# Kernel tuning notes

Hardware: AMD Instinct MI355X
Metric: run time of the kernel (lower is better)

Reference implementation:

```python
import jax, jax.numpy as jnp
import numpy as np

V, D, T_MAX, H, L = 32000, 1024, 1024, 16, 8
HD = D // H
DFF = 4 * D
EPS = 1e-5


def _pos_encoding(T, d_model, dtype=jnp.float32):
    pos = jnp.arange(T, dtype=jnp.float32)[:, None]                      # [T,1]
    div = jnp.exp(jnp.arange(0, d_model, 2, dtype=jnp.float32) * (-jnp.log(10000.0) / d_model))
    pe = jnp.zeros((T, d_model), dtype=jnp.float32)
    pe = pe.at[:, 0::2].set(jnp.sin(pos * div))
    pe = pe.at[:, 1::2].set(jnp.cos(pos * div))
    return pe.astype(dtype)


def _layernorm(x, g, b):
    mu = jnp.mean(x, axis=-1, keepdims=True)
    var = jnp.mean(jnp.square(x - mu), axis=-1, keepdims=True)
    return (x - mu) * jax.lax.rsqrt(var + EPS) * g + b


def setup_inputs() -> dict:
    key = jax.random.key(0)
    ks = jax.random.split(key, 9)
    s = 0.02
    return {
        "idx": jax.random.randint(ks[0], (2, 1024), 0, V),
        "embed": jax.random.normal(ks[1], (V, D), jnp.float32) * s,
        "Wqkv": jax.random.normal(ks[2], (L, D, 3 * D), jnp.float32) * s,
        "Wproj": jax.random.normal(ks[3], (L, D, D), jnp.float32) * s,
        "bproj": jnp.zeros((L, D), jnp.float32),
        "ln1_g": jnp.ones((L, D), jnp.float32),
        "ln1_b": jnp.zeros((L, D), jnp.float32),
        "ln2_g": jnp.ones((L, D), jnp.float32),
        "ln2_b": jnp.zeros((L, D), jnp.float32),
        "W1": jax.random.normal(ks[4], (L, D, DFF), jnp.float32) * s,
        "b1": jnp.zeros((L, DFF), jnp.float32),
        "W2": jax.random.normal(ks[5], (L, DFF, D), jnp.float32) * s,
        "b2": jnp.zeros((L, D), jnp.float32),
        "lnf_g": jnp.ones((D,), jnp.float32),
        "lnf_b": jnp.zeros((D,), jnp.float32),
        "Whead": jax.random.normal(ks[6], (D, V), jnp.float32) * s,
    }


def _attn(x, Wqkv, Wproj, bproj):
    B, T, C = x.shape
    qkv = (x @ Wqkv).reshape(B, T, 3, H, HD)
    q, k, v = [jnp.transpose(qkv[:, :, i], (0, 2, 1, 3)) for i in range(3)]  # [B,H,T,HD]
    scores = jnp.einsum('bhqd,bhkd->bhqk', q, k) * (HD ** -0.5)
    mask = jnp.tril(jnp.ones((T, T), dtype=bool))
    scores = jnp.where(mask, scores, -jnp.inf)
    w = jax.nn.softmax(scores, axis=-1)
    out = jnp.einsum('bhqk,bhkd->bhqd', w, v)
    out = jnp.transpose(out, (0, 2, 1, 3)).reshape(B, T, C)
    return out @ Wproj + bproj


def reference(idx, embed, Wqkv, Wproj, bproj, ln1_g, ln1_b, ln2_g, ln2_b,
              W1, b1, W2, b2, lnf_g, lnf_b, Whead):
    idx = idx[:, :T_MAX]
    T = idx.shape[1]
    x = embed[idx] + _pos_encoding(T, D)[None]          # [B,T,D]
    for l in range(L):
        x = x + _attn(_layernorm(x, ln1_g[l], ln1_b[l]), Wqkv[l], Wproj[l], bproj[l])
        h = _layernorm(x, ln2_g[l], ln2_b[l])
        x = x + jax.nn.relu(h @ W1[l] + b1[l]) @ W2[l] + b2[l]
    x = _layernorm(x, lnf_g, lnf_b)
    return x @ Whead                                     # [B,T,V]
```

## Files before the change

kernel.cpp:

```cpp
#include <hip/hip_runtime.h>
#include <cstddef>

#define DM    1024
#define TSEQ  1024
#define NB    2
#define NHEAD 16
#define HDIM  64
#define NLAYER 8
#define DFFN  4096
#define NVOC  32000
#define NROWS (NB*TSEQ)

typedef __attribute__((ext_vector_type(8))) short short8;
typedef __attribute__((ext_vector_type(4))) float f32x4;

static __device__ __forceinline__ unsigned short f2bf(float f) {
    union { float f; unsigned int u; } v; v.f = f;
    unsigned int r = v.u + 0x7FFF + ((v.u >> 16) & 1);
    return (unsigned short)(r >> 16);
}

static __device__ __forceinline__ void gload_lds16(const void* g, void* l) {
    __builtin_amdgcn_global_load_lds(
        (const __attribute__((address_space(1))) unsigned int*)g,
        (__attribute__((address_space(3))) unsigned int*)l, 16, 0, 0);
}

__global__ __launch_bounds__(256)
void embed_pos_k(const int* __restrict__ idx, const float* __restrict__ embed,
                 float* __restrict__ x)
{
    int row = blockIdx.x;
    int t   = row & (TSEQ - 1);
    int tid = threadIdx.x;
    int token = idx[row];
    const float* er = embed + (size_t)token * DM;
    float* xr = x + (size_t)row * DM;
    const float neg_ln1e4_over_d = -9.210340371976184f / (float)DM;
    for (int i = tid; i < DM; i += 256) {
        int half = i >> 1;
        float div = expf((float)(2 * half) * neg_ln1e4_over_d);
        float ang = (float)t * div;
        float pe = (i & 1) ? cosf(ang) : sinf(ang);
        xr[i] = er[i] + pe;
    }
}

__global__ __launch_bounds__(256)
void layernorm_k(const float* __restrict__ x, const float* __restrict__ g,
                 const float* __restrict__ b, unsigned short* __restrict__ y)
{
    int row = blockIdx.x;
    int tid = threadIdx.x;
    const float* xr = x + (size_t)row * DM;
    unsigned short* yr = y + (size_t)row * DM;
    float vals[4];
    float s = 0.f;
    #pragma unroll
    for (int i = 0; i < 4; ++i) { vals[i] = xr[tid + 256 * i]; s += vals[i]; }
    __shared__ float red[256];
    red[tid] = s; __syncthreads();
    for (int st = 128; st > 0; st >>= 1) {
        if (tid < st) red[tid] += red[tid + st];
        __syncthreads();
    }
    float mu = red[0] * (1.f / DM);
    __syncthreads();
    float v = 0.f;
    #pragma unroll
    for (int i = 0; i < 4; ++i) { float d = vals[i] - mu; v += d * d; }
    red[tid] = v; __syncthreads();
    for (int st = 128; st > 0; st >>= 1) {
        if (tid < st) red[tid] += red[tid + st];
        __syncthreads();
    }
    float rstd = rsqrtf(red[0] * (1.f / DM) + 1e-5f);
    #pragma unroll
    for (int i = 0; i < 4; ++i) {
        int c = tid + 256 * i;
        yr[c] = f2bf((vals[i] - mu) * rstd * g[c] + b[c]);
    }
}

__global__ __launch_bounds__(256)
void reduce_ln_k(const float* __restrict__ P, int nsplit, const float* __restrict__ bias,
                 float* __restrict__ X, const float* __restrict__ g,
                 const float* __restrict__ b, unsigned short* __restrict__ XN)
{
    const int row = blockIdx.x;
    const int tid = threadIdx.x;
    const size_t off4 = (size_t)row * 256 + tid;
    const size_t tot4 = (size_t)NROWS * 256;

    float4 v = *((const float4*)X + off4);
    float4 bb = *((const float4*)bias + tid);
    v.x += bb.x; v.y += bb.y; v.z += bb.z; v.w += bb.w;
    for (int s = 0; s < nsplit; ++s) {
        float4 p = *((const float4*)P + s * tot4 + off4);
        v.x += p.x; v.y += p.y; v.z += p.z; v.w += p.w;
    }
    *((float4*)X + off4) = v;

    __shared__ float red[256];
    red[tid] = v.x + v.y + v.z + v.w;
    __syncthreads();
    for (int st = 128; st > 0; st >>= 1) {
        if (tid < st) red[tid] += red[tid + st];
        __syncthreads();
    }
    float mu = red[0] * (1.f / DM);
    __syncthreads();
    float4 d = make_float4(v.x - mu, v.y - mu, v.z - mu, v.w - mu);
    red[tid] = d.x * d.x + d.y * d.y + d.z * d.z + d.w * d.w;
    __syncthreads();
    for (int st = 128; st > 0; st >>= 1) {
        if (tid < st) red[tid] += red[tid + st];
        __syncthreads();
    }
    float rstd = rsqrtf(red[0] * (1.f / DM) + 1e-5f);
    float4 gg = *((const float4*)g + tid);
    float4 bbn = *((const float4*)b + tid);
    unsigned short o[4];
    o[0] = f2bf(d.x * rstd * gg.x + bbn.x);
    o[1] = f2bf(d.y * rstd * gg.y + bbn.y);
    o[2] = f2bf(d.z * rstd * gg.z + bbn.z);
    o[3] = f2bf(d.w * rstd * gg.w + bbn.w);
    *(ushort4*)(XN + (size_t)row * DM + tid * 4) = *(ushort4*)o;
}

__global__ __launch_bounds__(256)
void convt_k(const float* __restrict__ src, unsigned short* __restrict__ dst,
             int K, int N)
{
    __shared__ __align__(16) unsigned short T[64][72];
    const int tid = threadIdx.x;
    const int n0 = blockIdx.x * 64, k0 = blockIdx.y * 64;
    const float* s = src + (size_t)blockIdx.z * K * N;
    unsigned short* d = dst + (size_t)blockIdx.z * K * N;
    #pragma unroll
    for (int q = 0; q < 4; ++q) {
        int f4 = tid + q * 256;
        int kk = f4 >> 4, nn = (f4 & 15) * 4;
        float4 v = *(const float4*)(s + (size_t)(k0 + kk) * N + n0 + nn);
        int swz = ((nn >> 2) & 7) << 3;
        T[nn + 0][kk ^ swz] = f2bf(v.x);
        T[nn + 1][kk ^ swz] = f2bf(v.y);
        T[nn + 2][kk ^ swz] = f2bf(v.z);
        T[nn + 3][kk ^ swz] = f2bf(v.w);
    }
    __syncthreads();
    #pragma unroll
    for (int q = 0; q < 2; ++q) {
        int s8 = tid + q * 256;
        int nn = s8 >> 3, kc = (s8 & 7) * 8;
        int swz = ((nn >> 2) & 7) << 3;
        *(short8*)(d + (size_t)(n0 + nn) * K + k0 + kc) =
            *(const short8*)&T[nn][kc ^ swz];
    }
}

template<bool OUT_BF16>
__global__ __launch_bounds__(512)
void gemm256(const unsigned short* __restrict__ A, const unsigned short* __restrict__ BT,
             const float* __restrict__ bias, void* __restrict__ Cout,
             int M, int N, int K, int relu)
{
    __shared__ __align__(16) unsigned short AS[3][256][64];
    __shared__ __align__(16) unsigned short BS[3][128][64];

    const int tid  = threadIdx.x;
    const int lane = tid & 63;
    const int w    = tid >> 6;
    const int wm = w >> 1, wn = w & 1;
    const int l16 = lane & 15, g = lane >> 4;

    const int nby = M / 256;
    const int nwg = nby * (N / 128);
    const int cpx = nwg >> 3;
    const int bid = (int)blockIdx.x;
    const int sbid = (bid & 7) * cpx + (bid >> 3);
    const int row0 = (sbid % nby) * 256;
    const int col0 = (sbid / nby) * 128;

    const int srow = tid >> 3;
    const int schunk = ((tid & 7) ^ (srow & 7)) << 3;
    const unsigned short* ga = A  + (size_t)(row0 + srow) * K + schunk;
    const unsigned short* gb = BT + (size_t)(col0 + srow) * K + schunk;
    const int NT = K >> 6;

    f32x4 acc[4][4] = {};

    #pragma unroll
    for (int t = 0; t < 2; ++t) {
        #pragma unroll
        for (int i = 0; i < 4; ++i)
            gload_lds16(ga + t * 64 + (size_t)(i * 64) * K,
                        (unsigned short*)AS[t] + i * 4096 + tid * 8);
        #pragma unroll
        for (int i = 0; i < 2; ++i)
            gload_lds16(gb + t * 64 + (size_t)(i * 64) * K,
                        (unsigned short*)BS[t] + i * 4096 + tid * 8);
    }
    asm volatile("s_waitcnt vmcnt(6)" ::: "memory");
    __builtin_amdgcn_s_barrier();

    for (int t = 0; t < NT; ++t) {
        const int rs = t % 3;
        if (t + 2 < NT) {
            const int ss = (t + 2) % 3;
            #pragma unroll
            for (int i = 0; i < 4; ++i)
                gload_lds16(ga + (t + 2) * 64 + (size_t)(i * 64) * K,
                            (unsigned short*)AS[ss] + i * 4096 + tid * 8);
            #pragma unroll
            for (int i = 0; i < 2; ++i)
                gload_lds16(gb + (t + 2) * 64 + (size_t)(i * 64) * K,
                            (unsigned short*)BS[ss] + i * 4096 + tid * 8);
        }
        #pragma unroll
        for (int s = 0; s < 2; ++s) {
            short8 af[4], bf[4];
            #pragma unroll
            for (int i = 0; i < 4; ++i) {
                const int ar = wm * 64 + i * 16 + l16;
                af[i] = *(const short8*)&AS[rs][ar][((((s << 2) | g) ^ (l16 & 7)) << 3)];
            }
            #pragma unroll
            for (int j = 0; j < 4; ++j) {
                const int br = wn * 64 + j * 16 + l16;
                bf[j] = *(const short8*)&BS[rs][br][((((s << 2) | g) ^ (l16 & 7)) << 3)];
            }
            __builtin_amdgcn_s_setprio(1);
            #pragma unroll
            for (int i = 0; i < 4; ++i)
                #pragma unroll
                for (int j = 0; j < 4; ++j)
                    acc[i][j] = __builtin_amdgcn_mfma_f32_16x16x32_bf16(af[i], bf[j], acc[i][j], 0, 0, 0);
            __builtin_amdgcn_s_setprio(0);
        }
        if (t + 2 < NT) { asm volatile("s_waitcnt vmcnt(6)" ::: "memory"); }
        else            { asm volatile("s_waitcnt vmcnt(0)" ::: "memory"); }
        __builtin_amdgcn_s_barrier();
    }

    #pragma unroll
    for (int i = 0; i < 4; ++i) {
        #pragma unroll
        for (int j = 0; j < 4; ++j) {
            #pragma unroll
            for (int r = 0; r < 4; ++r) {
                int row = row0 + wm * 64 + i * 16 + g * 4 + r;
                int col = col0 + wn * 64 + j * 16 + l16;
                float v = acc[i][j][r];
                if (bias) v += bias[col];
                if (relu) v = fmaxf(v, 0.f);
                if (OUT_BF16) ((unsigned short*)Cout)[(size_t)row * N + col] = f2bf(v);
                else          ((float*)Cout)[(size_t)row * N + col] = v;
            }
        }
    }
}

template<int BM, bool OUT_BF16>
__global__ __launch_bounds__(256)
void gemm_tn(const unsigned short* __restrict__ A, const unsigned short* __restrict__ BT,
             const float* __restrict__ bias, const float* __restrict__ residual,
             void* __restrict__ Cout, int M, int N, int K, int KS, int relu)
{
    constexpr int FR = BM / 32;
    constexpr int RPW = BM / 4;
    constexpr int NI = BM / 64;
    __shared__ __align__(16) unsigned short As[2][BM][32];
    __shared__ __align__(16) unsigned short Bs[2][BM][32];

    const int tid = threadIdx.x;
    const int lane = tid & 63;
    const int w = tid >> 6;
    const int wr = w >> 1, wc = w & 1;
    const int l16 = lane & 15, g = lane >> 4;

    const int nby = M / BM;
    const int nwg = (N / BM) * nby;
    const int cpx = nwg >> 3;
    const int bid = blockIdx.x;
    const int sbid = (bid & 7) * cpx + (bid >> 3);
    const int row0 = (sbid % nby) * BM;
    const int col0 = (sbid / nby) * BM;

    const int srow = w * RPW + (lane >> 2);
    const int scol = (((lane & 3) ^ ((lane >> 3) & 3)) << 3);
    const int rslot = ((g ^ ((l16 >> 1) & 3)) << 3);

    const unsigned short* ga = A  + (size_t)(row0 + srow) * KS + (size_t)blockIdx.y * K + scol;
    const unsigned short* gb = BT + (size_t)(col0 + srow) * KS + (size_t)blockIdx.y * K + scol;

    f32x4 acc[FR][FR] = {};

    #pragma unroll
    for (int i = 0; i < NI; ++i) {
        gload_lds16(ga + (size_t)(i * 16) * KS, &As[0][srow + i * 16][(lane & 3) << 3]);
        gload_lds16(gb + (size_t)(i * 16) * KS, &Bs[0][srow + i * 16][(lane & 3) << 3]);
    }
    __syncthreads();

    int cur = 0;
    for (int k0 = 0; k0 < K; k0 += 32) {
        if (k0 + 32 < K) {
            #pragma unroll
            for (int i = 0; i < NI; ++i) {
                gload_lds16(ga + k0 + 32 + (size_t)(i * 16) * KS, &As[cur ^ 1][srow + i * 16][(lane & 3) << 3]);
                gload_lds16(gb + k0 + 32 + (size_t)(i * 16) * KS, &Bs[cur ^ 1][srow + i * 16][(lane & 3) << 3]);
            }
        }
        short8 af[FR], bf[FR];
        #pragma unroll
        for (int i = 0; i < FR; ++i)
            af[i] = *(const short8*)&As[cur][wr * (BM / 2) + i * 16 + l16][rslot];
        #pragma unroll
        for (int j = 0; j < FR; ++j)
            bf[j] = *(const short8*)&Bs[cur][wc * (BM / 2) + j * 16 + l16][rslot];
        #pragma unroll
        for (int i = 0; i < FR; ++i)
            #pragma unroll
            for (int j = 0; j < FR; ++j)
                acc[i][j] = __builtin_amdgcn_mfma_f32_16x16x32_bf16(af[i], bf[j], acc[i][j], 0, 0, 0);
        __syncthreads();
        cur ^= 1;
    }

    float* Cf = (float*)Cout + (size_t)blockIdx.y * M * N;
    #pragma unroll
    for (int i = 0; i < FR; ++i) {
        #pragma unroll
        for (int j = 0; j < FR; ++j) {
            #pragma unroll
            for (int r = 0; r < 4; ++r) {
                int row = row0 + wr * (BM / 2) + i * 16 + g * 4 + r;
                int col = col0 + wc * (BM / 2) + j * 16 + l16;
                float v = acc[i][j][r];
                if (bias)     v += bias[col];
                if (residual) v += residual[(size_t)row * N + col];
                if (relu)     v = fmaxf(v, 0.f);
                if (OUT_BF16) ((unsigned short*)Cout)[(size_t)row * N + col] = f2bf(v);
                else          Cf[(size_t)row * N + col] = v;
            }
        }
    }
}

__global__ __launch_bounds__(256)
void attn_flash_k(const unsigned short* __restrict__ qkv, unsigned short* __restrict__ out)
{
    __shared__ unsigned short Ks[64][72];
    __shared__ unsigned short Vt[64][72];
    __shared__ unsigned short Ps[4][16][72];

    const int tid = threadIdx.x;
    const int lane = tid & 63;
    const int w = tid >> 6;
    const int l16 = lane & 15, g = lane >> 4;
    const int h = blockIdx.y;
    const int b = blockIdx.z;

    const size_t rstr = 3 * DM;
    const unsigned short* base = qkv + (size_t)b * TSEQ * rstr + h * HDIM;

    const int krow0 = tid >> 3, kcol = (tid & 7) * 8;
    const int vkv = tid & 63, vdg = tid >> 6;

    short8 kreg0, kreg1, vreg0, vreg1;

    #pragma unroll
    for (int pass = 0; pass < 2; ++pass) {
        const int qb = pass ? (15 - (int)blockIdx.x) : (int)blockIdx.x;
        const int q0 = qb * 64;
        const int nt = qb + 1;

        const int qrow_w = q0 + w * 16 + l16;
        short8 aq0 = *(const short8*)(base + (size_t)qrow_w * rstr + g * 8);
        short8 aq1 = *(const short8*)(base + (size_t)qrow_w * rstr + 32 + g * 8);

        f32x4 acc_o[4] = {};
        float m_r[4] = {-INFINITY, -INFINITY, -INFINITY, -INFINITY};
        float l_r[4] = {};

        {
            const unsigned short* kb = base + DM;
            kreg0 = *(const short8*)(kb + (size_t)krow0 * rstr + kcol);
            kreg1 = *(const short8*)(kb + (size_t)(32 + krow0) * rstr + kcol);
            const unsigned short* vsrc = base + (size_t)vkv * rstr + 2 * DM + vdg * 16;
            vreg0 = *(const short8*)vsrc;
            vreg1 = *(const short8*)(vsrc + 8);
        }

        for (int t = 0; t < nt; ++t) {
            *(short8*)&Ks[krow0][kcol] = kreg0;
            *(short8*)&Ks[32 + krow0][kcol] = kreg1;
            #pragma unroll
            for (int j = 0; j < 8; ++j) Vt[vdg * 16 + j][vkv] = (unsigned short)vreg0[j];
            #pragma unroll
            for (int j = 0; j < 8; ++j) Vt[vdg * 16 + 8 + j][vkv] = (unsigned short)vreg1[j];
            __syncthreads();

            if (t + 1 < nt) {
                const int kv0n = (t + 1) * 64;
                const unsigned short* kb = base + (size_t)kv0n * rstr + DM;
                kreg0 = *(const short8*)(kb + (size_t)krow0 * rstr + kcol);
                kreg1 = *(const short8*)(kb + (size_t)(32 + krow0) * rstr + kcol);
                const unsigned short* vsrc = base + (size_t)(kv0n + vkv) * rstr + 2 * DM + vdg * 16;
                vreg0 = *(const short8*)vsrc;
                vreg1 = *(const short8*)(vsrc + 8);
            }

            const int kv0 = t * 64;
            f32x4 acc_s[4] = {};
            #pragma unroll
            for (int ks = 0; ks < 4; ++ks) {
                short8 bk0 = *(const short8*)&Ks[ks * 16 + l16][g * 8];
                short8 bk1 = *(const short8*)&Ks[ks * 16 + l16][32 + g * 8];
                acc_s[ks] = __builtin_amdgcn_mfma_f32_16x16x32_bf16(aq0, bk0, acc_s[ks], 0, 0, 0);
                acc_s[ks] = __builtin_amdgcn_mfma_f32_16x16x32_bf16(aq1, bk1, acc_s[ks], 0, 0, 0);
            }
            const bool need_mask = (kv0 + 63 > q0 + w * 16);
            float alpha[4];
            #pragma unroll
            for (int r = 0; r < 4; ++r) {
                const int q_abs = q0 + w * 16 + g * 4 + r;
                float s[4];
                #pragma unroll
                for (int ks = 0; ks < 4; ++ks) {
                    s[ks] = acc_s[ks][r] * 0.125f;
                    if (need_mask && (kv0 + ks * 16 + l16 > q_abs)) s[ks] = -INFINITY;
                }
                float pm = fmaxf(fmaxf(s[0], s[1]), fmaxf(s[2], s[3]));
                #pragma unroll
                for (int msk = 1; msk <= 8; msk <<= 1)
                    pm = fmaxf(pm, __shfl_xor(pm, msk));
                float mnew = fmaxf(m_r[r], pm);
                alpha[r] = __expf(m_r[r] - mnew);
                m_r[r] = mnew;
                float p[4], psum = 0.f;
                #pragma unroll
                for (int ks = 0; ks < 4; ++ks) {
                    p[ks] = (s[ks] == -INFINITY) ? 0.f : __expf(s[ks] - mnew);
                    psum += p[ks];
                }
                #pragma unroll
                for (int msk = 1; msk <= 8; msk <<= 1)
                    psum += __shfl_xor(psum, msk);
                l_r[r] = l_r[r] * alpha[r] + psum;
                #pragma unroll
                for (int ks = 0; ks < 4; ++ks)
                    Ps[w][g * 4 + r][ks * 16 + l16] = f2bf(p[ks]);
            }
            #pragma unroll
            for (int ds = 0; ds < 4; ++ds)
                #pragma unroll
                for (int r = 0; r < 4; ++r)
                    acc_o[ds][r] *= alpha[r];
            short8 ap0 = *(const short8*)&Ps[w][l16][g * 8];
            short8 ap1 = *(const short8*)&Ps[w][l16][32 + g * 8];
            #pragma unroll
            for (int ds = 0; ds < 4; ++ds) {
                short8 bv0 = *(const short8*)&Vt[ds * 16 + l16][g * 8];
                short8 bv1 = *(const short8*)&Vt[ds * 16 + l16][32 + g * 8];
                acc_o[ds] = __builtin_amdgcn_mfma_f32_16x16x32_bf16(ap0, bv0, acc_o[ds], 0, 0, 0);
                acc_o[ds] = __builtin_amdgcn_mfma_f32_16x16x32_bf16(ap1, bv1, acc_o[ds], 0, 0, 0);
            }
            __syncthreads();
        }

        #pragma unroll
        for (int ds = 0; ds < 4; ++ds)
            #pragma unroll
            for (int r = 0; r < 4; ++r) {
                int row = q0 + w * 16 + g * 4 + r;
                out[((size_t)b * TSEQ + row) * DM + h * HDIM + ds * 16 + l16] =
                    f2bf(acc_o[ds][r] * (1.f / l_r[r]));
            }
    }
}

extern "C" void kernel_launch(void* const* d_in, const int* in_sizes, int n_in,
                              void* d_out, int out_size, void* d_ws, size_t ws_size,
                              hipStream_t stream)
{
    const int*   idx    = (const int*)  d_in[0];
    const float* embed  = (const float*)d_in[1];
    const float* Wqkv   = (const float*)d_in[2];
    const float* Wproj  = (const float*)d_in[3];
    const float* bproj  = (const float*)d_in[4];
    const float* ln1_g  = (const float*)d_in[5];
    const float* ln1_b  = (const float*)d_in[6];
    const float* ln2_g  = (const float*)d_in[7];
    const float* ln2_b  = (const float*)d_in[8];
    const float* W1     = (const float*)d_in[9];
    const float* b1     = (const float*)d_in[10];
    const float* W2     = (const float*)d_in[11];
    const float* b2     = (const float*)d_in[12];
    const float* lnf_g  = (const float*)d_in[13];
    const float* lnf_b  = (const float*)d_in[14];
    const float* Whead  = (const float*)d_in[15];
    float* out = (float*)d_out;

    float* X = (float*)d_ws;
    float* PK = X + (size_t)NROWS * DM;
    unsigned short* u = (unsigned short*)(PK + (size_t)4 * NROWS * DM);
    unsigned short* XN     = u;  u += (size_t)NROWS * DM;
    unsigned short* QKVb   = u;  u += (size_t)NROWS * 3 * DM;
    unsigned short* ATT    = u;  u += (size_t)NROWS * DM;
    unsigned short* FFH    = u;  u += (size_t)NROWS * DFFN;
    unsigned short* WqkvT  = u;  u += (size_t)NLAYER * 3 * DM * DM;
    unsigned short* WprojT = u;  u += (size_t)NLAYER * DM * DM;
    unsigned short* W1T    = u;  u += (size_t)NLAYER * DFFN * DM;
    unsigned short* W2T    = u;  u += (size_t)NLAYER * DM * DFFN;
    unsigned short* WheadT = u;  u += (size_t)NVOC * DM;

    convt_k<<<dim3(3 * DM / 64, DM / 64, NLAYER), 256, 0, stream>>>(Wqkv,  WqkvT,  DM,   3 * DM);
    convt_k<<<dim3(DM / 64,     DM / 64, NLAYER), 256, 0, stream>>>(Wproj, WprojT, DM,   DM);
    convt_k<<<dim3(DFFN / 64,   DM / 64, NLAYER), 256, 0, stream>>>(W1,    W1T,    DM,   DFFN);
    convt_k<<<dim3(DM / 64,   DFFN / 64, NLAYER), 256, 0, stream>>>(W2,    W2T,    DFFN, DM);
    convt_k<<<dim3(NVOC / 64,   DM / 64, 1),      256, 0, stream>>>(Whead, WheadT, DM,   NVOC);

    embed_pos_k<<<NROWS, 256, 0, stream>>>(idx, embed, X);
    layernorm_k<<<NROWS, 256, 0, stream>>>(X, ln1_g, ln1_b, XN);

    for (int l = 0; l < NLAYER; ++l) {
        const unsigned short* wqkvT_l  = WqkvT  + (size_t)l * 3 * DM * DM;
        const unsigned short* wprojT_l = WprojT + (size_t)l * DM * DM;
        const unsigned short* w1T_l    = W1T    + (size_t)l * DFFN * DM;
        const unsigned short* w2T_l    = W2T    + (size_t)l * DM * DFFN;
        const float* bproj_l = bproj + (size_t)l * DM;
        const float* b1_l = b1 + (size_t)l * DFFN;
        const float* b2_l = b2 + (size_t)l * DM;

        {
            int nwg = (NROWS / 256) * (3 * DM / 128);
            gemm256<true><<<nwg, 512, 0, stream>>>(XN, wqkvT_l, nullptr,
                                                   QKVb, NROWS, 3 * DM, DM, 0);
        }
        {
            dim3 grid(TSEQ / 128, NHEAD, NB);
            attn_flash_k<<<grid, 256, 0, stream>>>(QKVb, ATT);
        }
        {
            dim3 grid((NROWS / 128) * (DM / 128), 2);
            gemm_tn<128, false><<<grid, 256, 0, stream>>>(ATT, wprojT_l, nullptr, nullptr,
                                                          PK, NROWS, DM, 512, DM, 0);
            reduce_ln_k<<<NROWS, 256, 0, stream>>>(PK, 2, bproj_l, X,
                                                   ln2_g + (size_t)l * DM,
                                                   ln2_b + (size_t)l * DM, XN);
        }
        {
            int nwg = (NROWS / 256) * (DFFN / 128);
            gemm256<true><<<nwg, 512, 0, stream>>>(XN, w1T_l, b1_l,
                                                   FFH, NROWS, DFFN, DM, 1);
        }
        {
            dim3 grid((NROWS / 128) * (DM / 128), 4);
            gemm_tn<128, false><<<grid, 256, 0, stream>>>(FFH, w2T_l, nullptr, nullptr,
                                                          PK, NROWS, DM, 1024, DFFN, 0);
            const float* ng = (l + 1 < NLAYER) ? ln1_g + (size_t)(l + 1) * DM : lnf_g;
            const float* nb = (l + 1 < NLAYER) ? ln1_b + (size_t)(l + 1) * DM : lnf_b;
            reduce_ln_k<<<NROWS, 256, 0, stream>>>(PK, 4, b2_l, X, ng, nb, XN);
        }
    }

    {
        int nwg = (NROWS / 256) * (NVOC / 128);
        gemm256<false><<<nwg, 512, 0, stream>>>(XN, WheadT, nullptr,
                                                out, NROWS, NVOC, DM, 0);
    }
}
```

Measured before the change: 1.819 ms.

## Software-pipeline GEMM main loop into four MFMA phases with interleaved loads

```diff
diff --git a/kernel.cpp b/kernel.cpp
--- a/kernel.cpp
+++ b/kernel.cpp
@@ -188,6 +188,17 @@
     const unsigned short* gb = BT + (size_t)(col0 + srow) * K + schunk;
     const int NT = K >> 6;
 
+    const int ch0 = ((g ^ (l16 & 7)) << 3);
+    const int ch1 = (((4 | g) ^ (l16 & 7)) << 3);
+    const int ar0 = wm * 64 + 0  + l16;
+    const int ar1 = wm * 64 + 16 + l16;
+    const int ar2 = wm * 64 + 32 + l16;
+    const int ar3 = wm * 64 + 48 + l16;
+    const int br0 = wn * 64 + 0  + l16;
+    const int br1 = wn * 64 + 16 + l16;
+    const int br2 = wn * 64 + 32 + l16;
+    const int br3 = wn * 64 + 48 + l16;
+
     f32x4 acc[4][4] = {};
 
     #pragma unroll
@@ -204,43 +215,95 @@
     asm volatile("s_waitcnt vmcnt(6)" ::: "memory");
     __builtin_amdgcn_s_barrier();
 
+    short8 aE0 = *(const short8*)&AS[0][ar0][ch0];
+    short8 aE1 = *(const short8*)&AS[0][ar1][ch0];
+    short8 aO0, aO1;
+    short8 b0f[4], b1f[4];
+    b0f[0] = *(const short8*)&BS[0][br0][ch0];
+    b0f[1] = *(const short8*)&BS[0][br1][ch0];
+    b0f[2] = *(const short8*)&BS[0][br2][ch0];
+    b0f[3] = *(const short8*)&BS[0][br3][ch0];
+
     for (int t = 0; t < NT; ++t) {
         const int rs = t % 3;
-        if (t + 2 < NT) {
-            const int ss = (t + 2) % 3;
-            #pragma unroll
-            for (int i = 0; i < 4; ++i)
-                gload_lds16(ga + (t + 2) * 64 + (size_t)(i * 64) * K,
-                            (unsigned short*)AS[ss] + i * 4096 + tid * 8);
-            #pragma unroll
-            for (int i = 0; i < 2; ++i)
-                gload_lds16(gb + (t + 2) * 64 + (size_t)(i * 64) * K,
-                            (unsigned short*)BS[ss] + i * 4096 + tid * 8);
-        }
-        #pragma unroll
-        for (int s = 0; s < 2; ++s) {
-            short8 af[4], bf[4];
-            #pragma unroll
-            for (int i = 0; i < 4; ++i) {
-                const int ar = wm * 64 + i * 16 + l16;
-                af[i] = *(const short8*)&AS[rs][ar][((((s << 2) | g) ^ (l16 & 7)) << 3)];
-            }
-            #pragma unroll
-            for (int j = 0; j < 4; ++j) {
-                const int br = wn * 64 + j * 16 + l16;
-                bf[j] = *(const short8*)&BS[rs][br][((((s << 2) | g) ^ (l16 & 7)) << 3)];
-            }
-            __builtin_amdgcn_s_setprio(1);
-            #pragma unroll
-            for (int i = 0; i < 4; ++i)
-                #pragma unroll
-                for (int j = 0; j < 4; ++j)
-                    acc[i][j] = __builtin_amdgcn_mfma_f32_16x16x32_bf16(af[i], bf[j], acc[i][j], 0, 0, 0);
-            __builtin_amdgcn_s_setprio(0);
-        }
-        if (t + 2 < NT) { asm volatile("s_waitcnt vmcnt(6)" ::: "memory"); }
-        else            { asm volatile("s_waitcnt vmcnt(0)" ::: "memory"); }
+        const int ss = (t + 2) % 3;
+        const bool pf = (t + 2 < NT);
+        const unsigned short* gat = ga + (t + 2) * 64;
+        const unsigned short* gbt = gb + (t + 2) * 64;
+
+        aO0 = *(const short8*)&AS[rs][ar2][ch0];
+        aO1 = *(const short8*)&AS[rs][ar3][ch0];
+        if (pf) {
+            gload_lds16(gat,                      (unsigned short*)AS[ss] + 0 * 4096 + tid * 8);
+            gload_lds16(gat + (size_t)64 * K,     (unsigned short*)AS[ss] + 1 * 4096 + tid * 8);
+        }
+        __builtin_amdgcn_s_setprio(1);
+        #pragma unroll
+        for (int j = 0; j < 4; ++j)
+            acc[0][j] = __builtin_amdgcn_mfma_f32_16x16x32_bf16(aE0, b0f[j], acc[0][j], 0, 0, 0);
+        #pragma unroll
+        for (int j = 0; j < 4; ++j)
+            acc[1][j] = __builtin_amdgcn_mfma_f32_16x16x32_bf16(aE1, b0f[j], acc[1][j], 0, 0, 0);
+        __builtin_amdgcn_s_setprio(0);
         __builtin_amdgcn_s_barrier();
+
+        aE0 = *(const short8*)&AS[rs][ar0][ch1];
+        aE1 = *(const short8*)&AS[rs][ar1][ch1];
+        b1f[0] = *(const short8*)&BS[rs][br0][ch1];
+        b1f[1] = *(const short8*)&BS[rs][br1][ch1];
+        b1f[2] = *(const short8*)&BS[rs][br2][ch1];
+        b1f[3] = *(const short8*)&BS[rs][br3][ch1];
+        if (pf) {
+            gload_lds16(gat + (size_t)128 * K,    (unsigned short*)AS[ss] + 2 * 4096 + tid * 8);
+            gload_lds16(gat + (size_t)192 * K,    (unsigned short*)AS[ss] + 3 * 4096 + tid * 8);
+        }
+        __builtin_amdgcn_s_setprio(1);
+        #pragma unroll
+        for (int j = 0; j < 4; ++j)
+            acc[2][j] = __builtin_amdgcn_mfma_f32_16x16x32_bf16(aO0, b0f[j], acc[2][j], 0, 0, 0);
+        #pragma unroll
+        for (int j = 0; j < 4; ++j)
+            acc[3][j] = __builtin_amdgcn_mfma_f32_16x16x32_bf16(aO1, b0f[j], acc[3][j], 0, 0, 0);
+        __builtin_amdgcn_s_setprio(0);
+        __builtin_amdgcn_s_barrier();
+
+        aO0 = *(const short8*)&AS[rs][ar2][ch1];
+        aO1 = *(const short8*)&AS[rs][ar3][ch1];
+        if (pf)
+            gload_lds16(gbt,                      (unsigned short*)BS[ss] + 0 * 4096 + tid * 8);
+        __builtin_amdgcn_s_setprio(1);
+        #pragma unroll
+        for (int j = 0; j < 4; ++j)
+            acc[0][j] = __builtin_amdgcn_mfma_f32_16x16x32_bf16(aE0, b1f[j], acc[0][j], 0, 0, 0);
+        #pragma unroll
+        for (int j = 0; j < 4; ++j)
+            acc[1][j] = __builtin_amdgcn_mfma_f32_16x16x32_bf16(aE1, b1f[j], acc[1][j], 0, 0, 0);
+        __builtin_amdgcn_s_setprio(0);
+        __builtin_amdgcn_s_barrier();
+
+        if (pf)
+            gload_lds16(gbt + (size_t)64 * K,     (unsigned short*)BS[ss] + 1 * 4096 + tid * 8);
+        __builtin_amdgcn_s_setprio(1);
+        #pragma unroll
+        for (int j = 0; j < 4; ++j)
+            acc[2][j] = __builtin_amdgcn_mfma_f32_16x16x32_bf16(aO0, b1f[j], acc[2][j], 0, 0, 0);
+        #pragma unroll
+        for (int j = 0; j < 4; ++j)
+            acc[3][j] = __builtin_amdgcn_mfma_f32_16x16x32_bf16(aO1, b1f[j], acc[3][j], 0, 0, 0);
+        __builtin_amdgcn_s_setprio(0);
+        if (pf) { asm volatile("s_waitcnt vmcnt(6)" ::: "memory"); }
+        else    { asm volatile("s_waitcnt vmcnt(0)" ::: "memory"); }
+        __builtin_amdgcn_s_barrier();
+
+        if (t + 1 < NT) {
+            const int rs2 = (t + 1) % 3;
+            aE0 = *(const short8*)&AS[rs2][ar0][ch0];
+            aE1 = *(const short8*)&AS[rs2][ar1][ch0];
+            b0f[0] = *(const short8*)&BS[rs2][br0][ch0];
+            b0f[1] = *(const short8*)&BS[rs2][br1][ch0];
+            b0f[2] = *(const short8*)&BS[rs2][br2][ch0];
+            b0f[3] = *(const short8*)&BS[rs2][br3][ch0];
+        }
     }
 
     #pragma unroll
```

Result: no change. 1.807 ms (-0.6%).
